# Kernel optimization log

Measured on AMD Instinct MI355X. Metric: run time of the kernel, lower is better.

## Reference

```python
import jax, jax.numpy as jnp
import numpy as np

EPS = 1e-07  # DIoULoss eps


def setup_inputs() -> dict:
    key = jax.random.key(0)
    k1, k2, k3, k4, k5 = jax.random.split(key, 5)
    B, Q = 32, 131072
    # valid xyxy boxes: uniform centers in [0,100), sizes in [1,51)
    def make_boxes(kc, ks):
        c = jax.random.uniform(kc, (B, Q, 2), dtype=jnp.float32) * 100.0
        wh = jax.random.uniform(ks, (B, Q, 2), dtype=jnp.float32) * 50.0 + 1.0
        return jnp.concatenate([c - wh / 2, c + wh / 2], axis=-1)
    inputs = make_boxes(k1, k2)
    targets = make_boxes(k3, k4)
    mask = jax.random.randint(k5, (B, Q), 0, 2).astype(jnp.bool_)
    num_boxes = 2097152
    return {"inputs": inputs, "targets": targets, "mask": mask, "num_boxes": num_boxes}


def _diou_loss(b1, b2):
    # b1, b2: (N, 4) xyxy. Per-pair GIoU == diagonal of the original NxN matrix.
    a1 = (b1[:, 2] - b1[:, 0]) * (b1[:, 3] - b1[:, 1])
    a2 = (b2[:, 2] - b2[:, 0]) * (b2[:, 3] - b2[:, 1])
    lt = jnp.maximum(b1[:, :2], b2[:, :2])
    rb = jnp.minimum(b1[:, 2:], b2[:, 2:])
    wh = jnp.clip(rb - lt, 0.0)
    inter = wh[:, 0] * wh[:, 1]
    union = a1 + a2 - inter
    iou = inter / union
    lt_c = jnp.minimum(b1[:, :2], b2[:, :2])
    rb_c = jnp.maximum(b1[:, 2:], b2[:, 2:])
    wh_c = rb_c - lt_c  # boxes are valid so enclose extent >= 0
    area_c = wh_c[:, 0] * wh_c[:, 1]
    giou = iou - (area_c - union) / area_c
    # DIoU penalty: squared center distance / squared enclosing diagonal
    c1 = (b1[:, :2] + b1[:, 2:]) * 0.5
    c2 = (b2[:, :2] + b2[:, 2:]) * 0.5
    d2 = jnp.sum((c1 - c2) ** 2, axis=1)
    diag2 = wh_c[:, 0] ** 2 + wh_c[:, 1] ** 2
    diou = giou - d2 / (diag2 + EPS)
    return 1.0 - diou


def reference(inputs, targets, mask, num_boxes):
    B, Q, _ = inputs.shape
    loss = _diou_loss(inputs.reshape(-1, 4), targets.reshape(-1, 4)).reshape(B, Q)
    loss = loss * mask.astype(loss.dtype)
    # reduction='mean' with num_boxes provided -> sum / num_boxes
    return loss.sum() / num_boxes
```

## Files before the change

kernel.cpp:

```cpp
#include <hip/hip_runtime.h>

#define DIOU_EPS 1e-7f

constexpr int BLOCK = 256;
constexpr int GRID  = 1024;
constexpr int VPT   = 4;
constexpr int TILE  = BLOCK * VPT;

__device__ __forceinline__ float rcp_fast(float x) {
    return __builtin_amdgcn_rcpf(x);
}

__device__ __forceinline__ float diou_elem(float4 a, float4 b, int m) {
    float a1 = (a.z - a.x) * (a.w - a.y);
    float a2 = (b.z - b.x) * (b.w - b.y);

    float iw = fmaxf(fminf(a.z, b.z) - fmaxf(a.x, b.x), 0.0f);
    float ih = fmaxf(fminf(a.w, b.w) - fmaxf(a.y, b.y), 0.0f);
    float inter = iw * ih;
    float uni = a1 + a2 - inter;

    float wc = fmaxf(a.z, b.z) - fminf(a.x, b.x);
    float hc = fmaxf(a.w, b.w) - fminf(a.y, b.y);
    float area_c = wc * hc;

    float dx = (a.x + a.z - b.x - b.z) * 0.5f;
    float dy = (a.y + a.w - b.y - b.w) * 0.5f;
    float d2 = dx * dx + dy * dy;
    float diag2 = wc * wc + hc * hc;

    float loss = 2.0f - inter * rcp_fast(uni)
                      - uni   * rcp_fast(area_c)
                      + d2    * rcp_fast(diag2 + DIOU_EPS);

    return (m != 0) ? loss : 0.0f;
}

struct Tile {
    float4 A[VPT];
    float4 B[VPT];
    int4   M;
};

__device__ __forceinline__ void load_tile(const float4* __restrict__ boxes1,
                                          const float4* __restrict__ boxes2,
                                          const int4* __restrict__ mask4,
                                          long long e0, Tile& T) {
    #pragma unroll
    for (int j = 0; j < VPT; ++j) T.A[j] = boxes1[e0 + j];
    #pragma unroll
    for (int j = 0; j < VPT; ++j) T.B[j] = boxes2[e0 + j];
    T.M = mask4[e0 >> 2];
}

__global__ __launch_bounds__(BLOCK, 4) void diou_partial_kernel(
    const float4* __restrict__ boxes1,
    const float4* __restrict__ boxes2,
    const int* __restrict__ mask,
    float* __restrict__ ws,
    int n)
{
    const int t = threadIdx.x;
    const int4* mask4 = (const int4*)mask;
    const long long nfull = n / TILE;

    float acc = 0.0f;

    Tile cur, nxt;
    long long tb = blockIdx.x;
    bool any = tb < nfull;
    if (any) load_tile(boxes1, boxes2, mask4, tb * TILE + (long long)t * VPT, cur);

    while (any) {
        long long tn = tb + GRID;
        bool hn = tn < nfull;
        if (hn) load_tile(boxes1, boxes2, mask4, tn * TILE + (long long)t * VPT, nxt);

        int mm[VPT] = {cur.M.x, cur.M.y, cur.M.z, cur.M.w};
        #pragma unroll
        for (int j = 0; j < VPT; ++j) acc += diou_elem(cur.A[j], cur.B[j], mm[j]);

        cur = nxt;
        tb = tn;
        any = hn;
    }

    for (long long i = nfull * TILE + (long long)blockIdx.x * BLOCK + t; i < n;
         i += (long long)GRID * BLOCK)
        acc += diou_elem(boxes1[i], boxes2[i], mask[i]);

    #pragma unroll
    for (int off = 32; off > 0; off >>= 1)
        acc += __shfl_down(acc, off, 64);

    __shared__ float wsum[BLOCK / 64];
    if ((t & 63) == 0) wsum[t >> 6] = acc;
    __syncthreads();
    if (t == 0) ws[blockIdx.x] = wsum[0] + wsum[1] + wsum[2] + wsum[3];
}

__global__ __launch_bounds__(BLOCK) void finalize_kernel(
    const float* __restrict__ ws,
    const int* __restrict__ num_boxes,
    float* __restrict__ out)
{
    const int t = threadIdx.x;
    float a = 0.0f;
    #pragma unroll
    for (int i = 0; i < GRID / BLOCK; ++i) a += ws[i * BLOCK + t];

    #pragma unroll
    for (int off = 32; off > 0; off >>= 1)
        a += __shfl_down(a, off, 64);

    __shared__ float wsum[BLOCK / 64];
    if ((t & 63) == 0) wsum[t >> 6] = a;
    __syncthreads();
    if (t == 0)
        out[0] = (wsum[0] + wsum[1] + wsum[2] + wsum[3]) / (float)num_boxes[0];
}

extern "C" void kernel_launch(void* const* d_in, const int* in_sizes, int n_in,
                              void* d_out, int out_size, void* d_ws, size_t ws_size,
                              hipStream_t stream) {
    const float4* boxes1 = (const float4*)d_in[0];
    const float4* boxes2 = (const float4*)d_in[1];
    const int* mask = (const int*)d_in[2];
    const int* num_boxes = (const int*)d_in[3];

    float* out = (float*)d_out;
    float* partials = (float*)d_ws;
    int n = in_sizes[2];

    diou_partial_kernel<<<GRID, BLOCK, 0, stream>>>(boxes1, boxes2, mask, partials, n);
    finalize_kernel<<<1, BLOCK, 0, stream>>>(partials, num_boxes, out);
}
```

Measured before the change: 162.1 us.

## Use lane-strided coalesced loads, drop software prefetch, and double the grid

Each lane now loads elements strided by 64 within its wave, so every load instruction covers a contiguous span across the wave instead of each thread reading four adjacent float4s. The manual double-buffered prefetch is removed, and the grid doubles to 2048 blocks with a launch-bounds occupancy hint of 8, relying on more resident waves to hide latency. Indexing switches from 64-bit to 32-bit arithmetic. Without the prefetch, each thread has fewer loads in flight, so latency hiding depends on reaching the higher occupancy.

```diff
diff --git a/kernel.cpp b/kernel.cpp
--- a/kernel.cpp
+++ b/kernel.cpp
@@ -3,7 +3,8 @@
 #define DIOU_EPS 1e-7f
 
 constexpr int BLOCK = 256;
-constexpr int GRID  = 1024;
+constexpr int BPC   = 8;
+constexpr int GRID  = 256 * BPC;
 constexpr int VPT   = 4;
 constexpr int TILE  = BLOCK * VPT;
 
@@ -36,57 +37,38 @@
     return (m != 0) ? loss : 0.0f;
 }
 
-struct Tile {
-    float4 A[VPT];
-    float4 B[VPT];
-    int4   M;
-};
-
-__device__ __forceinline__ void load_tile(const float4* __restrict__ boxes1,
-                                          const float4* __restrict__ boxes2,
-                                          const int4* __restrict__ mask4,
-                                          long long e0, Tile& T) {
-    #pragma unroll
-    for (int j = 0; j < VPT; ++j) T.A[j] = boxes1[e0 + j];
-    #pragma unroll
-    for (int j = 0; j < VPT; ++j) T.B[j] = boxes2[e0 + j];
-    T.M = mask4[e0 >> 2];
-}
-
-__global__ __launch_bounds__(BLOCK, 4) void diou_partial_kernel(
+__global__ __launch_bounds__(BLOCK, BPC) void diou_partial_kernel(
     const float4* __restrict__ boxes1,
     const float4* __restrict__ boxes2,
     const int* __restrict__ mask,
     float* __restrict__ ws,
     int n)
 {
-    const int t = threadIdx.x;
-    const int4* mask4 = (const int4*)mask;
-    const long long nfull = n / TILE;
+    const int t    = threadIdx.x;
+    const int lane = t & 63;
+    const int wave = t >> 6;
+    const int nfull = n / TILE;
 
     float acc = 0.0f;
 
-    Tile cur, nxt;
-    long long tb = blockIdx.x;
-    bool any = tb < nfull;
-    if (any) load_tile(boxes1, boxes2, mask4, tb * TILE + (long long)t * VPT, cur);
+    for (int tb = blockIdx.x; tb < nfull; tb += GRID) {
+        const int base = tb * TILE + wave * (64 * VPT) + lane;
 
-    while (any) {
-        long long tn = tb + GRID;
-        bool hn = tn < nfull;
-        if (hn) load_tile(boxes1, boxes2, mask4, tn * TILE + (long long)t * VPT, nxt);
+        float4 A[VPT], B[VPT];
+        int    M[VPT];
+        #pragma unroll
+        for (int j = 0; j < VPT; ++j) A[j] = boxes1[base + j * 64];
+        #pragma unroll
+        for (int j = 0; j < VPT; ++j) B[j] = boxes2[base + j * 64];
+        #pragma unroll
+        for (int j = 0; j < VPT; ++j) M[j] = mask[base + j * 64];
 
-        int mm[VPT] = {cur.M.x, cur.M.y, cur.M.z, cur.M.w};
         #pragma unroll
-        for (int j = 0; j < VPT; ++j) acc += diou_elem(cur.A[j], cur.B[j], mm[j]);
-
-        cur = nxt;
-        tb = tn;
-        any = hn;
+        for (int j = 0; j < VPT; ++j) acc += diou_elem(A[j], B[j], M[j]);
     }
 
-    for (long long i = nfull * TILE + (long long)blockIdx.x * BLOCK + t; i < n;
-         i += (long long)GRID * BLOCK)
+    for (int i = nfull * TILE + blockIdx.x * BLOCK + t; i < n;
+         i += GRID * BLOCK)
         acc += diou_elem(boxes1[i], boxes2[i], mask[i]);
 
     #pragma unroll
@@ -94,7 +76,7 @@
         acc += __shfl_down(acc, off, 64);
 
     __shared__ float wsum[BLOCK / 64];
-    if ((t & 63) == 0) wsum[t >> 6] = acc;
+    if (lane == 0) wsum[wave] = acc;
     __syncthreads();
     if (t == 0) ws[blockIdx.x] = wsum[0] + wsum[1] + wsum[2] + wsum[3];
 }
```

Result: no change. 164.8 us (+1.6%).
